# Kernel optimization log

Hardware: AMD Instinct MI355X
Metric: run time of the kernel (lower is better)

## Reference

```python
import jax, jax.numpy as jnp
from jax import lax
import numpy as np

B, T, C, W = 128, 64, 64, 27
H, K = 128, 3
EPS = 1e-5


def _conv1d(x, w, b):
    # x: (N, Cin, W), w: (Cout, Cin, K) -> (N, Cout, W), 'same' padding
    y = lax.conv_general_dilated(x, w, (1,), 'SAME', dimension_numbers=('NCH', 'OIH', 'NCH'))
    return y + b[None, :, None]


def _mish(x):
    return x * jnp.tanh(jax.nn.softplus(x))


def _gru_layer(x_seq, act_seq, gw, gb, cw, cb, aw, ab, bn_g, bn_b):
    # x_seq: (T, B, Cin, W); act_seq: (T, B, 8, W)
    Hd = bn_g.shape[0]

    def step(h, xa):
        x, a = xa
        gates = _conv1d(jnp.concatenate([x, h], axis=1), gw, gb)  # (B, 2H, W)
        reset = jax.nn.sigmoid(gates[:, :Hd])
        update = jax.nn.sigmoid(gates[:, Hd:])
        cnm = _conv1d(jnp.concatenate([x, reset * h], axis=1), cw, cb) + _conv1d(a, aw, ab)
        pre = _mish((1.0 - update) * h + update * cnm)
        # BatchNorm1d (training mode): per-channel stats over (batch, width)
        mean = pre.mean(axis=(0, 2), keepdims=True)
        var = pre.var(axis=(0, 2), keepdims=True)
        h_next = bn_g[None, :, None] * (pre - mean) * lax.rsqrt(var + EPS) + bn_b[None, :, None]
        return h_next, h_next

    h0 = jnp.zeros((x_seq.shape[1], Hd, x_seq.shape[3]), dtype=x_seq.dtype)
    _, ys = lax.scan(step, h0, (x_seq, act_seq))
    return ys  # (T, B, H, W)


def setup_inputs():
    key = jax.random.key(0)
    ks = jax.random.split(key, 16)
    s = 0.05
    d = {}
    d['input_tensor'] = jax.random.normal(ks[0], (B, T, C, W), dtype=jnp.float32)
    # layer 0 (cur_input_dim = C)
    d['gates_w0'] = jax.random.normal(ks[1], (2 * H, C + H, K)) * s
    d['gates_b0'] = jnp.zeros((2 * H,))
    d['can_w0'] = jax.random.normal(ks[2], (H, C + H, K)) * s
    d['can_b0'] = jnp.zeros((H,))
    d['cond_w0'] = jax.random.normal(ks[3], (H, 8, K)) * s
    d['cond_b0'] = jnp.zeros((H,))
    d['bn_g0'] = jnp.ones((H,))
    d['bn_b0'] = jnp.zeros((H,))
    # layer 1 (cur_input_dim = H)
    d['gates_w1'] = jax.random.normal(ks[4], (2 * H, H + H, K)) * s
    d['gates_b1'] = jnp.zeros((2 * H,))
    d['can_w1'] = jax.random.normal(ks[5], (H, H + H, K)) * s
    d['can_b1'] = jnp.zeros((H,))
    d['cond_w1'] = jax.random.normal(ks[6], (H, 8, K)) * s
    d['cond_b1'] = jnp.zeros((H,))
    d['bn_g1'] = jnp.ones((H,))
    d['bn_b1'] = jnp.zeros((H,))
    # concentrate linear: (27*H) -> 1
    d['conc_w'] = jax.random.normal(ks[7], (1, W * H)) * s
    d['conc_b'] = jnp.zeros((1,))
    return d


def reference(input_tensor, gates_w0, gates_b0, can_w0, can_b0, cond_w0, cond_b0, bn_g0, bn_b0,
              gates_w1, gates_b1, can_w1, can_b1, cond_w1, cond_b1, bn_g1, bn_b1, conc_w, conc_b):
    x_t = jnp.transpose(input_tensor, (1, 0, 2, 3))  # (T, B, C, W)
    act_t = x_t[:, :, -8:, :]                        # (T, B, 8, W)
    h1 = _gru_layer(x_t, act_t, gates_w0, gates_b0, can_w0, can_b0, cond_w0, cond_b0, bn_g0, bn_b0)
    h2 = _gru_layer(h1, act_t, gates_w1, gates_b1, can_w1, can_b1, cond_w1, cond_b1, bn_g1, bn_b1)
    # (T, B, H, W) -> (B, T, H*W)
    out = jnp.transpose(h2, (1, 0, 2, 3)).reshape(input_tensor.shape[0], input_tensor.shape[1], -1)
    reward = out @ conc_w.T[:, 0] + conc_b[0]        # (B, T)
    return 0.99 * (reward[:, -1] - reward[:, -2])
```

## Files before the change

### kernel.cpp

```cpp
#include <hip/hip_runtime.h>
#include <math.h>

#define Bn 128
#define Tn 64
#define Cn 64
#define Wn 27
#define Hn 128
#define EPSf 1e-5f
#define NBWf 3456.0f

__device__ __forceinline__ void bn_coef(const float* __restrict__ sums,
                                        const float* __restrict__ g,
                                        const float* __restrict__ b,
                                        int c, float& sc, float& sh) {
  float s1 = sums[2 * c], s2 = sums[2 * c + 1];
  float mean = s1 * (1.0f / NBWf);
  float var = s2 * (1.0f / NBWf) - mean * mean;
  sc = g[c] * rsqrtf(var + EPSf);
  sh = b[c] - mean * sc;
}

__device__ __forceinline__ float sigm(float x) {
  return 1.0f / (1.0f + __expf(-x));
}

template <int IC, bool XN, bool HV>
__global__ __launch_bounds__(512, 1) void k_step(
    const float* __restrict__ in, int t,
    const float* __restrict__ xpre, const float* __restrict__ xsums,
    const float* __restrict__ xg, const float* __restrict__ xb,
    const float* __restrict__ hpre, const float* __restrict__ hsums,
    const float* __restrict__ hg, const float* __restrict__ hb,
    const float* __restrict__ wtg, const float* __restrict__ gbias,
    const float* __restrict__ wtc, const float* __restrict__ cbias,
    const float* __restrict__ wta, const float* __restrict__ abias,
    float* __restrict__ pre_out, float* __restrict__ sums_out) {
  constexpr int ROWS = IC + 136;
  __shared__ float lx[ROWS * 17 + 8];
  __shared__ float lrh[128 * 17 + 8];
  __shared__ float lu[128 * 17 + 8];
  __shared__ float red1[512];
  __shared__ float red2[512];
  const int b = blockIdx.x;
  const int y = blockIdx.y;
  const int wlo = y ? 12 : -1;
  const int tid = threadIdx.x;

  for (int r = tid; r < ROWS; r += 512) {
    float sc = 1.f, sh = 0.f;
    const float* src = nullptr;
    if (r < IC) {
      if (XN) {
        bn_coef(xsums, xg, xb, r, sc, sh);
        src = xpre + ((size_t)b * Hn + r) * Wn;
      } else {
        src = in + (((size_t)b * Tn + t) * Cn + r) * Wn;
      }
    } else if (r < IC + 128) {
      if (HV) {
        bn_coef(hsums, hg, hb, r - IC, sc, sh);
        src = hpre + ((size_t)b * Hn + (r - IC)) * Wn;
      }
    } else {
      src = in + (((size_t)b * Tn + t) * Cn + 56 + (r - IC - 128)) * Wn;
    }
    float* dst = &lx[r * 17];
#pragma unroll
    for (int c = 0; c < 17; ++c) {
      int w = wlo + c;
      float v = 0.f;
      if (src && (unsigned)w < 27u) v = src[w] * sc + sh;
      dst[c] = v;
    }
  }
  __syncthreads();

  {
    const int GP = y ? 14 : 15;
    const int och = tid & 255;
    const int seg = tid >> 8;
    const int c0 = 1 + seg * 8;
    float acc[8] = {0, 0, 0, 0, 0, 0, 0, 0};
    const float* wp = wtg + och;
    const int rows = HV ? IC + 128 : IC;
#pragma unroll 2
    for (int i = 0; i < rows; ++i) {
      float w0 = wp[0], w1 = wp[256], w2 = wp[512];
      wp += 768;
      const float* row = &lx[i * 17 + c0 - 1];
      float xv[10];
#pragma unroll
      for (int j = 0; j < 10; ++j) xv[j] = row[j];
#pragma unroll
      for (int j = 0; j < 8; ++j)
        acc[j] = fmaf(w2, xv[j + 2], fmaf(w1, xv[j + 1], fmaf(w0, xv[j], acc[j])));
    }
    float bias = gbias[och];
    if (och < 128) {
#pragma unroll
      for (int j = 0; j < 8; ++j) {
        int c = c0 + j;
        float g = sigm(acc[j] + bias);
        float hn = lx[(IC + och) * 17 + c];
        lrh[och * 17 + c] = (c <= GP) ? g * hn : 0.f;
      }
      if (seg == 0) lrh[och * 17] = 0.f;
    } else {
      const int ch = och - 128;
#pragma unroll
      for (int j = 0; j < 8; ++j) {
        int c = c0 + j;
        if (c <= GP) lu[ch * 17 + c] = sigm(acc[j] + bias);
      }
    }
  }
  __syncthreads();

  {
    const int ch = tid & 127;
    const int seg = tid >> 7;
    const int c0 = (y ? 2 : 1) + seg * 4;
    float acc[4] = {0, 0, 0, 0};
    const float* wp = wtc + ch;
#pragma unroll 2
    for (int i = 0; i < IC; ++i) {
      float w0 = wp[0], w1 = wp[128], w2 = wp[256];
      wp += 384;
      const float* row = &lx[i * 17 + c0 - 1];
      float xv[6];
#pragma unroll
      for (int j = 0; j < 6; ++j) xv[j] = row[j];
#pragma unroll
      for (int j = 0; j < 4; ++j)
        acc[j] = fmaf(w2, xv[j + 2], fmaf(w1, xv[j + 1], fmaf(w0, xv[j], acc[j])));
    }
    if (HV) {
#pragma unroll 2
      for (int i = 0; i < 128; ++i) {
        float w0 = wp[0], w1 = wp[128], w2 = wp[256];
        wp += 384;
        const float* row = &lrh[i * 17 + c0 - 1];
        float xv[6];
#pragma unroll
        for (int j = 0; j < 6; ++j) xv[j] = row[j];
#pragma unroll
        for (int j = 0; j < 4; ++j)
          acc[j] = fmaf(w2, xv[j + 2], fmaf(w1, xv[j + 1], fmaf(w0, xv[j], acc[j])));
      }
    }
    {
      const float* wap = wta + ch;
#pragma unroll
      for (int i = 0; i < 8; ++i) {
        float w0 = wap[0], w1 = wap[128], w2 = wap[256];
        wap += 384;
        const float* row = &lx[(IC + 128 + i) * 17 + c0 - 1];
        float xv[6];
#pragma unroll
        for (int j = 0; j < 6; ++j) xv[j] = row[j];
#pragma unroll
        for (int j = 0; j < 4; ++j)
          acc[j] = fmaf(w2, xv[j + 2], fmaf(w1, xv[j + 1], fmaf(w0, xv[j], acc[j])));
      }
    }
    const float cb = cbias[ch] + abias[ch];
    float s1 = 0.f, s2 = 0.f;
#pragma unroll
    for (int j = 0; j < 4; ++j) {
      int c = c0 + j;
      if (c <= 14) {
        float u = lu[ch * 17 + c];
        float hn = lx[(IC + ch) * 17 + c];
        float z = (1.f - u) * hn + u * (acc[j] + cb);
        float pv;
        if (z > 20.f) {
          pv = z;
        } else {
          float q = 1.f + __expf(z);
          float q2 = q * q;
          pv = z * (q2 - 1.f) / (q2 + 1.f);
        }
        pre_out[((size_t)b * Hn + ch) * Wn + (wlo + c)] = pv;
        s1 += pv;
        s2 += pv * pv;
      }
    }
    red1[tid] = s1;
    red2[tid] = s2;
  }
  __syncthreads();
  if (tid < 128) {
    float a1 = red1[tid] + red1[tid + 128] + red1[tid + 256] + red1[tid + 384];
    float a2 = red2[tid] + red2[tid + 128] + red2[tid + 256] + red2[tid + 384];
    atomicAdd(&sums_out[2 * tid], a1);
    atomicAdd(&sums_out[2 * tid + 1], a2);
  }
}

__global__ __launch_bounds__(256) void k_out(
    const float* __restrict__ p63, const float* __restrict__ s63,
    const float* __restrict__ p62, const float* __restrict__ s62,
    const float* __restrict__ g, const float* __restrict__ bb,
    const float* __restrict__ concw, float* __restrict__ out) {
  int b = blockIdx.x, tid = threadIdx.x;
  float acc = 0.f;
  for (int idx = tid; idx < Hn * Wn; idx += 256) {
    int o = idx / Wn;
    float sc3, sh3, sc2, sh2;
    bn_coef(s63, g, bb, o, sc3, sh3);
    bn_coef(s62, g, bb, o, sc2, sh2);
    float v3 = p63[(size_t)b * Hn * Wn + idx] * sc3 + sh3;
    float v2 = p62[(size_t)b * Hn * Wn + idx] * sc2 + sh2;
    acc += (v3 - v2) * concw[idx];
  }
  __shared__ float red[256];
  red[tid] = acc;
  __syncthreads();
  for (int s = 128; s > 0; s >>= 1) {
    if (tid < s) red[tid] += red[tid + s];
    __syncthreads();
  }
  if (tid == 0) out[b] = 0.99f * red[0];
}

__global__ void k_twt(const float* __restrict__ src, float* __restrict__ dst,
                      int M, int IC) {
  int idx = blockIdx.x * 256 + threadIdx.x;
  int total = M * IC * 3;
  if (idx >= total) return;
  int o = idx % M;
  int rem = idx / M;
  int i = rem / 3, k = rem - 3 * i;
  dst[idx] = src[((size_t)o * IC + i) * 3 + k];
}

extern "C" void kernel_launch(void* const* d_in, const int* in_sizes, int n_in,
                              void* d_out, int out_size, void* d_ws,
                              size_t ws_size, hipStream_t stream) {
  const float* in = (const float*)d_in[0];
  const float* gw0 = (const float*)d_in[1];
  const float* gb0 = (const float*)d_in[2];
  const float* cw0 = (const float*)d_in[3];
  const float* cb0 = (const float*)d_in[4];
  const float* aw0 = (const float*)d_in[5];
  const float* ab0 = (const float*)d_in[6];
  const float* bg0 = (const float*)d_in[7];
  const float* bb0 = (const float*)d_in[8];
  const float* gw1 = (const float*)d_in[9];
  const float* gb1 = (const float*)d_in[10];
  const float* cw1 = (const float*)d_in[11];
  const float* cb1 = (const float*)d_in[12];
  const float* aw1 = (const float*)d_in[13];
  const float* ab1 = (const float*)d_in[14];
  const float* bg1 = (const float*)d_in[15];
  const float* bb1 = (const float*)d_in[16];
  const float* concw = (const float*)d_in[17];
  float* out = (float*)d_out;

  float* ws = (float*)d_ws;
  size_t off = 0;
  float* wt_g0 = ws + off; off += 576 * 256;
  float* wt_c0 = ws + off; off += 576 * 128;
  float* wt_a0 = ws + off; off += 24 * 128;
  float* wt_g1 = ws + off; off += 768 * 256;
  float* wt_c1 = ws + off; off += 768 * 128;
  float* wt_a1 = ws + off; off += 24 * 128;
  const size_t PRE = (size_t)Bn * Hn * Wn;
  float* pre1[2] = {ws + off, ws + off + PRE}; off += 2 * PRE;
  float* pre2[2] = {ws + off, ws + off + PRE}; off += 2 * PRE;
  float* sums = ws + off; off += 2 * 64 * 128 * 2;
  if (ws_size < off * sizeof(float)) return;

  hipMemsetAsync(sums, 0, 2 * 64 * 128 * 2 * sizeof(float), stream);

  auto tw = [&](const float* s, float* d, int M, int IC) {
    int tot = M * IC * 3;
    k_twt<<<(tot + 255) / 256, 256, 0, stream>>>(s, d, M, IC);
  };
  tw(gw0, wt_g0, 256, 192);
  tw(cw0, wt_c0, 128, 192);
  tw(aw0, wt_a0, 128, 8);
  tw(gw1, wt_g1, 256, 256);
  tw(cw1, wt_c1, 128, 256);
  tw(aw1, wt_a1, 128, 8);

  auto sl = [&](int layer, int t) {
    return sums + ((size_t)(layer * 64 + t) * 128) * 2;
  };

  dim3 grd(Bn, 2);
  for (int t = 0; t < 64; ++t) {
    if (t == 0) {
      k_step<64, false, false><<<grd, 512, 0, stream>>>(
          in, t, nullptr, nullptr, nullptr, nullptr,
          nullptr, nullptr, nullptr, nullptr,
          wt_g0, gb0, wt_c0, cb0, wt_a0, ab0, pre1[0], sl(0, 0));
      k_step<128, true, false><<<grd, 512, 0, stream>>>(
          in, t, pre1[0], sl(0, 0), bg0, bb0,
          nullptr, nullptr, nullptr, nullptr,
          wt_g1, gb1, wt_c1, cb1, wt_a1, ab1, pre2[0], sl(1, 0));
    } else {
      k_step<64, false, true><<<grd, 512, 0, stream>>>(
          in, t, nullptr, nullptr, nullptr, nullptr,
          pre1[(t + 1) & 1], sl(0, t - 1), bg0, bb0,
          wt_g0, gb0, wt_c0, cb0, wt_a0, ab0, pre1[t & 1], sl(0, t));
      k_step<128, true, true><<<grd, 512, 0, stream>>>(
          in, t, pre1[t & 1], sl(0, t), bg0, bb0,
          pre2[(t + 1) & 1], sl(1, t - 1), bg1, bb1,
          wt_g1, gb1, wt_c1, cb1, wt_a1, ab1, pre2[t & 1], sl(1, t));
    }
  }
  k_out<<<Bn, 256, 0, stream>>>(pre2[1], sl(1, 63), pre2[0], sl(1, 62),
                                bg1, bb1, concw, out);
}
```

Before: 6.795 ms.

## Fuse all timesteps into one persistent kernel with grid barriers and pipelined layers

Replaces the 128 per-step launches with one persistent kernel of 256 blocks. Blocks 0-127 run layer 0 and blocks 128-255 run layer 1 one step behind, separated by an atomic-counter grid barrier. Each block now covers the full width of 27 with swizzled float4 LDS rows, splits the input channels across lanes and reduces them with shuffles. It also folds the output reduction into the same kernel. The aim is to remove launch overhead and let the two layers overlap, at the cost of relying on all 256 blocks being co-resident (a deadlock risk) and on heavy register use with 27 accumulators.

```diff
diff --git a/kernel.cpp b/kernel.cpp
--- a/kernel.cpp
+++ b/kernel.cpp
@@ -8,6 +8,23 @@
 #define Hn 128
 #define EPSf 1e-5f
 #define NBWf 3456.0f
+
+struct Params {
+  const float* in;
+  const float* wt_g0; const float* gb0;
+  const float* wt_c0; const float* cb0;
+  const float* wt_a0; const float* ab0;
+  const float* bg0; const float* bb0;
+  const float* wt_g1; const float* gb1;
+  const float* wt_c1; const float* cb1;
+  const float* wt_a1; const float* ab1;
+  const float* bg1; const float* bb1;
+  const float* concw;
+  float* pre1a; float* pre1b; float* pre2a; float* pre2b;
+  float* sums;
+  unsigned* cnt;
+  float* out;
+};
 
 __device__ __forceinline__ void bn_coef(const float* __restrict__ sums,
                                         const float* __restrict__ g,
@@ -24,154 +41,159 @@
   return 1.0f / (1.0f + __expf(-x));
 }
 
-template <int IC, bool XN, bool HV>
-__global__ __launch_bounds__(512, 1) void k_step(
-    const float* __restrict__ in, int t,
-    const float* __restrict__ xpre, const float* __restrict__ xsums,
+__device__ __forceinline__ int swz(int row, int c) {
+  return row * 32 + ((((c >> 2) ^ (row & 7)) & 7) << 2) + (c & 3);
+}
+
+__device__ __forceinline__ void conv_row(const float* __restrict__ rowbase,
+                                         int sw, float w0, float w1, float w2,
+                                         float* __restrict__ acc) {
+  const float4* rp = (const float4*)rowbase;
+  float xa[16];
+  {
+    float4 v0 = rp[0 ^ sw];
+    float4 v1 = rp[1 ^ sw];
+    float4 v2 = rp[2 ^ sw];
+    float4 v3 = rp[3 ^ sw];
+    xa[0] = v0.x; xa[1] = v0.y; xa[2] = v0.z; xa[3] = v0.w;
+    xa[4] = v1.x; xa[5] = v1.y; xa[6] = v1.z; xa[7] = v1.w;
+    xa[8] = v2.x; xa[9] = v2.y; xa[10] = v2.z; xa[11] = v2.w;
+    xa[12] = v3.x; xa[13] = v3.y; xa[14] = v3.z; xa[15] = v3.w;
+  }
+#pragma unroll
+  for (int c = 1; c <= 14; ++c)
+    acc[c - 1] = fmaf(w2, xa[c + 1], fmaf(w1, xa[c], fmaf(w0, xa[c - 1], acc[c - 1])));
+  float xc[15];
+  xc[0] = xa[14]; xc[1] = xa[15];
+  {
+    float4 v4 = rp[4 ^ sw];
+    float4 v5 = rp[5 ^ sw];
+    float4 v6 = rp[6 ^ sw];
+    float4 v7 = rp[7 ^ sw];
+    xc[2] = v4.x; xc[3] = v4.y; xc[4] = v4.z; xc[5] = v4.w;
+    xc[6] = v5.x; xc[7] = v5.y; xc[8] = v5.z; xc[9] = v5.w;
+    xc[10] = v6.x; xc[11] = v6.y; xc[12] = v6.z; xc[13] = v6.w;
+    xc[14] = v7.x;
+  }
+#pragma unroll
+  for (int k = 0; k < 13; ++k)
+    acc[14 + k] = fmaf(w2, xc[k + 2], fmaf(w1, xc[k + 1], fmaf(w0, xc[k], acc[14 + k])));
+}
+
+template <int IC, bool XN>
+__device__ void step_body(const Params& p, int b, int t, bool hv,
+    const float* __restrict__ xpre, const float* __restrict__ xs,
     const float* __restrict__ xg, const float* __restrict__ xb,
-    const float* __restrict__ hpre, const float* __restrict__ hsums,
+    const float* __restrict__ hpre, const float* __restrict__ hs,
     const float* __restrict__ hg, const float* __restrict__ hb,
     const float* __restrict__ wtg, const float* __restrict__ gbias,
     const float* __restrict__ wtc, const float* __restrict__ cbias,
     const float* __restrict__ wta, const float* __restrict__ abias,
-    float* __restrict__ pre_out, float* __restrict__ sums_out) {
+    float* __restrict__ pre_out, float* __restrict__ sums_out,
+    float* lx, float* lrh, float* lu) {
+  const int tid = threadIdx.x;
   constexpr int ROWS = IC + 136;
-  __shared__ float lx[ROWS * 17 + 8];
-  __shared__ float lrh[128 * 17 + 8];
-  __shared__ float lu[128 * 17 + 8];
-  __shared__ float red1[512];
-  __shared__ float red2[512];
-  const int b = blockIdx.x;
-  const int y = blockIdx.y;
-  const int wlo = y ? 12 : -1;
-  const int tid = threadIdx.x;
-
-  for (int r = tid; r < ROWS; r += 512) {
+  for (int r = tid; r < ROWS; r += 1024) {
     float sc = 1.f, sh = 0.f;
     const float* src = nullptr;
     if (r < IC) {
       if (XN) {
-        bn_coef(xsums, xg, xb, r, sc, sh);
+        bn_coef(xs, xg, xb, r, sc, sh);
         src = xpre + ((size_t)b * Hn + r) * Wn;
       } else {
-        src = in + (((size_t)b * Tn + t) * Cn + r) * Wn;
+        src = p.in + (((size_t)b * Tn + t) * Cn + r) * Wn;
       }
     } else if (r < IC + 128) {
-      if (HV) {
-        bn_coef(hsums, hg, hb, r - IC, sc, sh);
+      if (hv) {
+        bn_coef(hs, hg, hb, r - IC, sc, sh);
         src = hpre + ((size_t)b * Hn + (r - IC)) * Wn;
       }
     } else {
-      src = in + (((size_t)b * Tn + t) * Cn + 56 + (r - IC - 128)) * Wn;
-    }
-    float* dst = &lx[r * 17];
-#pragma unroll
-    for (int c = 0; c < 17; ++c) {
-      int w = wlo + c;
-      float v = 0.f;
-      if (src && (unsigned)w < 27u) v = src[w] * sc + sh;
-      dst[c] = v;
+      src = p.in + (((size_t)b * Tn + t) * Cn + 56 + (r - IC - 128)) * Wn;
+    }
+    lx[swz(r, 0)] = 0.f;
+    lx[swz(r, 28)] = 0.f; lx[swz(r, 29)] = 0.f;
+    lx[swz(r, 30)] = 0.f; lx[swz(r, 31)] = 0.f;
+    if (src) {
+      for (int w = 0; w < Wn; ++w) lx[swz(r, 1 + w)] = src[w] * sc + sh;
+    } else {
+      for (int w = 0; w < Wn; ++w) lx[swz(r, 1 + w)] = 0.f;
     }
   }
   __syncthreads();
-
   {
-    const int GP = y ? 14 : 15;
-    const int och = tid & 255;
-    const int seg = tid >> 8;
-    const int c0 = 1 + seg * 8;
-    float acc[8] = {0, 0, 0, 0, 0, 0, 0, 0};
-    const float* wp = wtg + och;
-    const int rows = HV ? IC + 128 : IC;
-#pragma unroll 2
-    for (int i = 0; i < rows; ++i) {
+    const int rc = tid & 3;
+    const int och = tid >> 2;
+    float acc[27];
+#pragma unroll
+    for (int j = 0; j < 27; ++j) acc[j] = 0.f;
+    const int rows = hv ? IC + 128 : IC;
+    for (int i = rc; i < rows; i += 4) {
+      const float* wp = wtg + (size_t)3 * i * 256 + och;
       float w0 = wp[0], w1 = wp[256], w2 = wp[512];
-      wp += 768;
-      const float* row = &lx[i * 17 + c0 - 1];
-      float xv[10];
-#pragma unroll
-      for (int j = 0; j < 10; ++j) xv[j] = row[j];
-#pragma unroll
-      for (int j = 0; j < 8; ++j)
-        acc[j] = fmaf(w2, xv[j + 2], fmaf(w1, xv[j + 1], fmaf(w0, xv[j], acc[j])));
-    }
-    float bias = gbias[och];
-    if (och < 128) {
-#pragma unroll
-      for (int j = 0; j < 8; ++j) {
-        int c = c0 + j;
-        float g = sigm(acc[j] + bias);
-        float hn = lx[(IC + och) * 17 + c];
-        lrh[och * 17 + c] = (c <= GP) ? g * hn : 0.f;
-      }
-      if (seg == 0) lrh[och * 17] = 0.f;
-    } else {
-      const int ch = och - 128;
-#pragma unroll
-      for (int j = 0; j < 8; ++j) {
-        int c = c0 + j;
-        if (c <= GP) lu[ch * 17 + c] = sigm(acc[j] + bias);
+      conv_row(lx + i * 32, i & 7, w0, w1, w2, acc);
+    }
+#pragma unroll
+    for (int j = 0; j < 27; ++j) {
+      acc[j] += __shfl_xor(acc[j], 1);
+      acc[j] += __shfl_xor(acc[j], 2);
+    }
+    if (rc == 0) {
+      const float bias = gbias[och];
+      if (och < 128) {
+        lrh[swz(och, 0)] = 0.f;
+        lrh[swz(och, 28)] = 0.f; lrh[swz(och, 29)] = 0.f;
+        lrh[swz(och, 30)] = 0.f; lrh[swz(och, 31)] = 0.f;
+#pragma unroll
+        for (int c = 1; c <= 27; ++c) {
+          float gv = sigm(acc[c - 1] + bias);
+          lrh[swz(och, c)] = gv * lx[swz(IC + och, c)];
+        }
+      } else {
+        const int ch = och - 128;
+#pragma unroll
+        for (int c = 1; c <= 27; ++c)
+          lu[ch * 27 + (c - 1)] = sigm(acc[c - 1] + bias);
       }
     }
   }
   __syncthreads();
-
   {
-    const int ch = tid & 127;
-    const int seg = tid >> 7;
-    const int c0 = (y ? 2 : 1) + seg * 4;
-    float acc[4] = {0, 0, 0, 0};
-    const float* wp = wtc + ch;
-#pragma unroll 2
-    for (int i = 0; i < IC; ++i) {
-      float w0 = wp[0], w1 = wp[128], w2 = wp[256];
-      wp += 384;
-      const float* row = &lx[i * 17 + c0 - 1];
-      float xv[6];
-#pragma unroll
-      for (int j = 0; j < 6; ++j) xv[j] = row[j];
-#pragma unroll
-      for (int j = 0; j < 4; ++j)
-        acc[j] = fmaf(w2, xv[j + 2], fmaf(w1, xv[j + 1], fmaf(w0, xv[j], acc[j])));
-    }
-    if (HV) {
-#pragma unroll 2
-      for (int i = 0; i < 128; ++i) {
-        float w0 = wp[0], w1 = wp[128], w2 = wp[256];
-        wp += 384;
-        const float* row = &lrh[i * 17 + c0 - 1];
-        float xv[6];
-#pragma unroll
-        for (int j = 0; j < 6; ++j) xv[j] = row[j];
-#pragma unroll
-        for (int j = 0; j < 4; ++j)
-          acc[j] = fmaf(w2, xv[j + 2], fmaf(w1, xv[j + 1], fmaf(w0, xv[j], acc[j])));
+    const int rc8 = tid & 7;
+    const int ch = tid >> 3;
+    float acc[27];
+#pragma unroll
+    for (int j = 0; j < 27; ++j) acc[j] = 0.f;
+    for (int i = rc8; i < IC; i += 8) {
+      const float* wp = wtc + (size_t)3 * i * 128 + ch;
+      conv_row(lx + i * 32, i & 7, wp[0], wp[128], wp[256], acc);
+    }
+    if (hv) {
+      for (int i = rc8; i < 128; i += 8) {
+        const float* wp = wtc + (size_t)3 * (IC + i) * 128 + ch;
+        conv_row(lrh + i * 32, i & 7, wp[0], wp[128], wp[256], acc);
       }
     }
     {
-      const float* wap = wta + ch;
-#pragma unroll
-      for (int i = 0; i < 8; ++i) {
-        float w0 = wap[0], w1 = wap[128], w2 = wap[256];
-        wap += 384;
-        const float* row = &lx[(IC + 128 + i) * 17 + c0 - 1];
-        float xv[6];
-#pragma unroll
-        for (int j = 0; j < 6; ++j) xv[j] = row[j];
-#pragma unroll
-        for (int j = 0; j < 4; ++j)
-          acc[j] = fmaf(w2, xv[j + 2], fmaf(w1, xv[j + 1], fmaf(w0, xv[j], acc[j])));
-      }
-    }
-    const float cb = cbias[ch] + abias[ch];
-    float s1 = 0.f, s2 = 0.f;
-#pragma unroll
-    for (int j = 0; j < 4; ++j) {
-      int c = c0 + j;
-      if (c <= 14) {
-        float u = lu[ch * 17 + c];
-        float hn = lx[(IC + ch) * 17 + c];
-        float z = (1.f - u) * hn + u * (acc[j] + cb);
+      const int i = rc8;
+      const float* wp = wta + (size_t)3 * i * 128 + ch;
+      const int r = IC + 128 + i;
+      conv_row(lx + r * 32, r & 7, wp[0], wp[128], wp[256], acc);
+    }
+#pragma unroll
+    for (int j = 0; j < 27; ++j) {
+      acc[j] += __shfl_xor(acc[j], 1);
+      acc[j] += __shfl_xor(acc[j], 2);
+      acc[j] += __shfl_xor(acc[j], 4);
+    }
+    if (rc8 == 0) {
+      const float cb = cbias[ch] + abias[ch];
+      float s1 = 0.f, s2 = 0.f;
+#pragma unroll
+      for (int c = 1; c <= 27; ++c) {
+        float u = lu[ch * 27 + (c - 1)];
+        float hn = lx[swz(IC + ch, c)];
+        float z = (1.f - u) * hn + u * (acc[c - 1] + cb);
         float pv;
         if (z > 20.f) {
           pv = z;
@@ -180,47 +202,88 @@
           float q2 = q * q;
           pv = z * (q2 - 1.f) / (q2 + 1.f);
         }
-        pre_out[((size_t)b * Hn + ch) * Wn + (wlo + c)] = pv;
+        pre_out[((size_t)b * Hn + ch) * Wn + (c - 1)] = pv;
         s1 += pv;
         s2 += pv * pv;
       }
-    }
-    red1[tid] = s1;
-    red2[tid] = s2;
-  }
+      atomicAdd(&sums_out[2 * ch], s1);
+      atomicAdd(&sums_out[2 * ch + 1], s2);
+    }
+  }
+}
+
+__device__ __forceinline__ void gbar(unsigned* cnt, unsigned target) {
   __syncthreads();
-  if (tid < 128) {
-    float a1 = red1[tid] + red1[tid + 128] + red1[tid + 256] + red1[tid + 384];
-    float a2 = red2[tid] + red2[tid + 128] + red2[tid + 256] + red2[tid + 384];
-    atomicAdd(&sums_out[2 * tid], a1);
-    atomicAdd(&sums_out[2 * tid + 1], a2);
-  }
-}
-
-__global__ __launch_bounds__(256) void k_out(
-    const float* __restrict__ p63, const float* __restrict__ s63,
-    const float* __restrict__ p62, const float* __restrict__ s62,
-    const float* __restrict__ g, const float* __restrict__ bb,
-    const float* __restrict__ concw, float* __restrict__ out) {
-  int b = blockIdx.x, tid = threadIdx.x;
-  float acc = 0.f;
-  for (int idx = tid; idx < Hn * Wn; idx += 256) {
-    int o = idx / Wn;
-    float sc3, sh3, sc2, sh2;
-    bn_coef(s63, g, bb, o, sc3, sh3);
-    bn_coef(s62, g, bb, o, sc2, sh2);
-    float v3 = p63[(size_t)b * Hn * Wn + idx] * sc3 + sh3;
-    float v2 = p62[(size_t)b * Hn * Wn + idx] * sc2 + sh2;
-    acc += (v3 - v2) * concw[idx];
-  }
-  __shared__ float red[256];
-  red[tid] = acc;
+  if (threadIdx.x == 0) {
+    __threadfence();
+    atomicAdd(cnt, 1u);
+    while (__hip_atomic_load(cnt, __ATOMIC_RELAXED, __HIP_MEMORY_SCOPE_AGENT) < target) {
+      __builtin_amdgcn_s_sleep(8);
+    }
+    __threadfence();
+  }
   __syncthreads();
-  for (int s = 128; s > 0; s >>= 1) {
-    if (tid < s) red[tid] += red[tid + s];
+}
+
+__global__ __launch_bounds__(1024, 4) void k_all(Params p) {
+  __shared__ __align__(16) float lx[264 * 32];
+  __shared__ __align__(16) float lrh[128 * 32];
+  __shared__ float lu[128 * 27];
+  const int bid = blockIdx.x;
+  const bool L1b = bid >= 128;
+  const int b = L1b ? bid - 128 : bid;
+  float* pre1[2] = {p.pre1a, p.pre1b};
+  float* pre2[2] = {p.pre2a, p.pre2b};
+  for (int ph = 0; ph < 65; ++ph) {
+    if (!L1b) {
+      if (ph < 64) {
+        const int t = ph;
+        const bool hv = t > 0;
+        step_body<Cn, false>(p, b, t, hv,
+            nullptr, nullptr, nullptr, nullptr,
+            hv ? pre1[(t - 1) & 1] : nullptr,
+            hv ? p.sums + (size_t)(t - 1) * 256 : nullptr, p.bg0, p.bb0,
+            p.wt_g0, p.gb0, p.wt_c0, p.cb0, p.wt_a0, p.ab0,
+            pre1[t & 1], p.sums + (size_t)t * 256, lx, lrh, lu);
+      }
+    } else {
+      if (ph >= 1) {
+        const int t = ph - 1;
+        const bool hv = t > 0;
+        step_body<Hn, true>(p, b, t, hv,
+            pre1[t & 1], p.sums + (size_t)t * 256, p.bg0, p.bb0,
+            hv ? pre2[(t - 1) & 1] : nullptr,
+            hv ? p.sums + (size_t)(64 + t - 1) * 256 : nullptr, p.bg1, p.bb1,
+            p.wt_g1, p.gb1, p.wt_c1, p.cb1, p.wt_a1, p.ab1,
+            pre2[t & 1], p.sums + (size_t)(64 + t) * 256, lx, lrh, lu);
+      }
+    }
+    gbar(p.cnt, (unsigned)(ph + 1) * 256u);
+  }
+  if (!L1b) {
+    const float* p63 = pre2[1];
+    const float* p62 = pre2[0];
+    const float* s63 = p.sums + (size_t)(64 + 63) * 256;
+    const float* s62 = p.sums + (size_t)(64 + 62) * 256;
+    const int tid = threadIdx.x;
+    float acc = 0.f;
+    for (int idx = tid; idx < Hn * Wn; idx += 1024) {
+      int o = idx / Wn;
+      float sc3, sh3, sc2, sh2;
+      bn_coef(s63, p.bg1, p.bb1, o, sc3, sh3);
+      bn_coef(s62, p.bg1, p.bb1, o, sc2, sh2);
+      float v3 = p63[(size_t)b * Hn * Wn + idx] * sc3 + sh3;
+      float v2 = p62[(size_t)b * Hn * Wn + idx] * sc2 + sh2;
+      acc += (v3 - v2) * p.concw[idx];
+    }
+    lx[tid] = acc;
     __syncthreads();
-  }
-  if (tid == 0) out[b] = 0.99f * red[0];
+    for (int s = 512; s > 0; s >>= 1) {
+      if (tid < s) lx[tid] += lx[tid + s];
+      __syncthreads();
+    }
+    if (tid == 0) p.out[b] = 0.99f * lx[0];
+  }
 }
 
 __global__ void k_twt(const float* __restrict__ src, float* __restrict__ dst,
@@ -266,12 +329,15 @@
   float* wt_c1 = ws + off; off += 768 * 128;
   float* wt_a1 = ws + off; off += 24 * 128;
   const size_t PRE = (size_t)Bn * Hn * Wn;
-  float* pre1[2] = {ws + off, ws + off + PRE}; off += 2 * PRE;
-  float* pre2[2] = {ws + off, ws + off + PRE}; off += 2 * PRE;
-  float* sums = ws + off; off += 2 * 64 * 128 * 2;
+  float* pre1a = ws + off; off += PRE;
+  float* pre1b = ws + off; off += PRE;
+  float* pre2a = ws + off; off += PRE;
+  float* pre2b = ws + off; off += PRE;
+  float* sums = ws + off; off += 2 * 64 * 256;
+  unsigned* cnt = (unsigned*)(ws + off); off += 16;
   if (ws_size < off * sizeof(float)) return;
 
-  hipMemsetAsync(sums, 0, 2 * 64 * 128 * 2 * sizeof(float), stream);
+  hipMemsetAsync(sums, 0, (2 * 64 * 256 + 16) * sizeof(float), stream);
 
   auto tw = [&](const float* s, float* d, int M, int IC) {
     int tot = M * IC * 3;
@@ -284,32 +350,20 @@
   tw(cw1, wt_c1, 128, 256);
   tw(aw1, wt_a1, 128, 8);
 
-  auto sl = [&](int layer, int t) {
-    return sums + ((size_t)(layer * 64 + t) * 128) * 2;
-  };
-
-  dim3 grd(Bn, 2);
-  for (int t = 0; t < 64; ++t) {
-    if (t == 0) {
-      k_step<64, false, false><<<grd, 512, 0, stream>>>(
-          in, t, nullptr, nullptr, nullptr, nullptr,
-          nullptr, nullptr, nullptr, nullptr,
-          wt_g0, gb0, wt_c0, cb0, wt_a0, ab0, pre1[0], sl(0, 0));
-      k_step<128, true, false><<<grd, 512, 0, stream>>>(
-          in, t, pre1[0], sl(0, 0), bg0, bb0,
-          nullptr, nullptr, nullptr, nullptr,
-          wt_g1, gb1, wt_c1, cb1, wt_a1, ab1, pre2[0], sl(1, 0));
-    } else {
-      k_step<64, false, true><<<grd, 512, 0, stream>>>(
-          in, t, nullptr, nullptr, nullptr, nullptr,
-          pre1[(t + 1) & 1], sl(0, t - 1), bg0, bb0,
-          wt_g0, gb0, wt_c0, cb0, wt_a0, ab0, pre1[t & 1], sl(0, t));
-      k_step<128, true, true><<<grd, 512, 0, stream>>>(
-          in, t, pre1[t & 1], sl(0, t), bg0, bb0,
-          pre2[(t + 1) & 1], sl(1, t - 1), bg1, bb1,
-          wt_g1, gb1, wt_c1, cb1, wt_a1, ab1, pre2[t & 1], sl(1, t));
-    }
-  }
-  k_out<<<Bn, 256, 0, stream>>>(pre2[1], sl(1, 63), pre2[0], sl(1, 62),
-                                bg1, bb1, concw, out);
-}
+  Params prm;
+  prm.in = in;
+  prm.wt_g0 = wt_g0; prm.gb0 = gb0;
+  prm.wt_c0 = wt_c0; prm.cb0 = cb0;
+  prm.wt_a0 = wt_a0; prm.ab0 = ab0;
+  prm.bg0 = bg0; prm.bb0 = bb0;
+  prm.wt_g1 = wt_g1; prm.gb1 = gb1;
+  prm.wt_c1 = wt_c1; prm.cb1 = cb1;
+  prm.wt_a1 = wt_a1; prm.ab1 = ab1;
+  prm.bg1 = bg1; prm.bb1 = bb1;
+  prm.concw = concw;
+  prm.pre1a = pre1a; prm.pre1b = pre1b;
+  prm.pre2a = pre2a; prm.pre2b = pre2b;
+  prm.sums = sums; prm.cnt = cnt; prm.out = out;
+
+  k_all<<<256, 1024, 0, stream>>>(prm);
+}
```

After: 7.402 ms. +8.9%, slower.
